# Optimization experiments

Measured on AMD Instinct MI355X. Metric: run time of the kernel, lower is better.

The kernel has to match this reference:

```python
import jax, jax.numpy as jnp
import numpy as np

B, T, C = 2, 2048, 2048
H, KVH, HD = 16, 4, 128
EPS = 1e-5


def _rope(x, cos, sin):
    # x: (B,T,h,HD); cos/sin: (1,T,1,HD//2); halves-split rotary (not interleaved)
    d = x.shape[-1] // 2
    x1, x2 = x[..., :d], x[..., d:]
    return jnp.concatenate([x1 * cos + x2 * sin, -x1 * sin + x2 * cos], axis=-1)


def _rms_norm(x, eps=EPS):
    return x * jax.lax.rsqrt(jnp.mean(x * x, axis=-1, keepdims=True) + eps)


def setup_inputs() -> dict:
    key = jax.random.key(0)
    ks = jax.random.split(key, 5)
    x = jax.random.normal(ks[0], (B, T, C), dtype=jnp.float32)
    # realistic RoPE tables (theta=10000)
    inv_freq = 1.0 / (10000.0 ** (np.arange(HD // 2, dtype=np.float32) / (HD // 2)))
    t = np.arange(T, dtype=np.float32)
    freqs = np.outer(t, inv_freq)  # (T, HD/2)
    cos = jnp.asarray(np.cos(freqs))[None, :, None, :]
    sin = jnp.asarray(np.sin(freqs))[None, :, None, :]
    s = 0.02
    wq = jax.random.normal(ks[1], (C, H * HD), dtype=jnp.float32) * s
    wk = jax.random.normal(ks[2], (C, KVH * HD), dtype=jnp.float32) * s
    wv = jax.random.normal(ks[3], (C, KVH * HD), dtype=jnp.float32) * s
    wo = jax.random.normal(ks[4], (H * HD, C), dtype=jnp.float32) * s
    return {"x": x, "cos": cos, "sin": sin, "wq": wq, "wk": wk, "wv": wv, "wo": wo, "window_size": 0}


def reference(x, cos, sin, wq, wk, wv, wo, window_size):
    # window_size is unused on the training (no-kv-cache) path, as in the source.
    b, t, _ = x.shape
    q = (x @ wq).reshape(b, t, H, HD)
    k = (x @ wk).reshape(b, t, KVH, HD)
    v = (x @ wv).reshape(b, t, KVH, HD)
    q = _rms_norm(_rope(q, cos, sin))
    k = _rms_norm(_rope(k, cos, sin))
    n_rep = H // KVH
    # grouped-query attention without materializing repeated K/V
    qg = q.reshape(b, t, KVH, n_rep, HD)
    scale = 1.0 / jnp.sqrt(jnp.float32(HD))
    scores = jnp.einsum('btkrd,bskd->bkrts', qg, k) * scale  # (B,KVH,n_rep,T,T)
    causal = jnp.tril(jnp.ones((t, t), dtype=bool))
    scores = jnp.where(causal, scores, jnp.finfo(scores.dtype).min)
    attn = jax.nn.softmax(scores, axis=-1)
    y = jnp.einsum('bkrts,bskd->btkrd', attn, v).reshape(b, t, H * HD)
    return y @ wo
```

## Files before the change

### kernel.cpp

```cpp
#include <hip/hip_runtime.h>
#include <hip/hip_bf16.h>


using bf16 = __bf16;
typedef __bf16 bf16x8 __attribute__((ext_vector_type(8)));
typedef __bf16 bf16x4 __attribute__((ext_vector_type(4)));
typedef float  f32x4  __attribute__((ext_vector_type(4)));

__device__ __forceinline__ void gload_lds16(const void* g, void* l) {
  __builtin_amdgcn_global_load_lds(
      (const __attribute__((address_space(1))) unsigned int*)g,
      (__attribute__((address_space(3))) unsigned int*)l, 16, 0, 0);
}

__device__ __forceinline__ unsigned pack2(float a, float b) {
  unsigned short ua = __builtin_bit_cast(unsigned short, (bf16)a);
  unsigned short ub = __builtin_bit_cast(unsigned short, (bf16)b);
  return ((unsigned)ub << 16) | ua;
}

#define SBAR() do { __builtin_amdgcn_s_barrier(); \
                    __builtin_amdgcn_sched_barrier(0); } while (0)
#define VMCNT(n) asm volatile("s_waitcnt vmcnt(" #n ")" ::: "memory")

__global__ __launch_bounds__(256) void k_cvt_bf16(const float* __restrict__ src,
                                                  bf16* __restrict__ dst) {
  const int i = blockIdx.x * 256 + threadIdx.x;
  f32x4 v = ((const f32x4*)src)[i];
  bf16x4 o;
  o[0] = (bf16)v[0]; o[1] = (bf16)v[1]; o[2] = (bf16)v[2]; o[3] = (bf16)v[3];
  ((bf16x4*)dst)[i] = o;
}

__global__ __launch_bounds__(256) void k_transpose_cvt(const float* __restrict__ src,
                                                       bf16* __restrict__ dst,
                                                       int R, int C) {
  __shared__ float tile[32][33];
  const int c0 = blockIdx.x * 32, r0 = blockIdx.y * 32;
  const int tx = threadIdx.x & 31, ty = threadIdx.x >> 5;
#pragma unroll
  for (int j = 0; j < 32; j += 8)
    tile[ty + j][tx] = src[(size_t)(r0 + ty + j) * C + c0 + tx];
  __syncthreads();
#pragma unroll
  for (int j = 0; j < 32; j += 8)
    dst[(size_t)(c0 + ty + j) * R + r0 + tx] = (bf16)tile[tx][ty + j];
}

template <int BM, bool OUT_BF16>
__global__ __launch_bounds__(512, 1) void k_gemm32(
    const bf16* __restrict__ A,
    const bf16* __restrict__ B0, const bf16* __restrict__ B1,
    const bf16* __restrict__ B2, int nb1, int nb2,
    void* __restrict__ Cout, int K, int Ntot) {
  constexpr int MR  = BM / 32;
  constexpr int ACH = BM / 128;
  __shared__ __align__(16) bf16 As[4][BM * 32];
  __shared__ __align__(16) bf16 Bs[4][256 * 32];
  const int nb = blockIdx.x, mb = blockIdx.y;
  const bf16* Bt; int nloc;
  if (nb < nb1)      { Bt = B0; nloc = nb; }
  else if (nb < nb2) { Bt = B1; nloc = nb - nb1; }
  else               { Bt = B2; nloc = nb - nb2; }
  const int tid = threadIdx.x;
  const int w = tid >> 6, lane = tid & 63;
  const int wm = w >> 2, wn = w & 3;
  const int l16 = lane & 15, lq = lane >> 4;
  const int sr4 = lane >> 2, sc4 = lane & 3;
  const bf16* Ag = A  + (size_t)mb * BM * K;
  const bf16* Bg = Bt + (size_t)nloc * 256 * K;

  f32x4 acc[MR][4] = {};

  auto stage = [&](int t) {
    const int buf = t & 3;
    const int k0 = t * 32;
#pragma unroll
    for (int i = 0; i < 2; ++i) {
      const int r = i * 128 + w * 16 + sr4;
      const int cg = sc4 ^ ((r >> 1) & 3);
      gload_lds16(Bg + (size_t)r * K + k0 + cg * 8,
                  &Bs[buf][(i * 128 + w * 16) * 32]);
    }
#pragma unroll
    for (int i = 0; i < ACH; ++i) {
      const int r = i * 128 + w * 16 + sr4;
      const int cg = sc4 ^ ((r >> 1) & 3);
      gload_lds16(Ag + (size_t)r * K + k0 + cg * 8,
                  &As[buf][(i * 128 + w * 16) * 32]);
    }
  };

  const int NT = K / 32;
  stage(0); stage(1); stage(2);
  if (BM == 256) VMCNT(8); else VMCNT(6);
  SBAR();

  for (int t = 0; t < NT; ++t) {
    const int buf = t & 3;
    if (t + 3 < NT) stage(t + 3);
    const int rem = NT - 1 - t;
    if (BM == 256) {
      if (rem >= 3)      VMCNT(12);
      else if (rem == 2) VMCNT(8);
      else if (rem == 1) VMCNT(4);
      else               VMCNT(0);
    } else {
      if (rem >= 3)      VMCNT(9);
      else if (rem == 2) VMCNT(6);
      else if (rem == 1) VMCNT(3);
      else               VMCNT(0);
    }
    SBAR();
    bf16x8 bfr[4], af[MR];
#pragma unroll
    for (int j = 0; j < 4; ++j) {
      const int rb = wn * 64 + j * 16 + l16;
      bfr[j] = *(const bf16x8*)((const char*)&Bs[buf][0] + rb * 64 +
                                ((lq ^ ((rb >> 1) & 3)) << 4));
    }
#pragma unroll
    for (int i = 0; i < MR; ++i) {
      const int ra = wm * (BM / 2) + i * 16 + l16;
      af[i] = *(const bf16x8*)((const char*)&As[buf][0] + ra * 64 +
                               ((lq ^ ((ra >> 1) & 3)) << 4));
    }
    __builtin_amdgcn_s_setprio(1);
#pragma unroll
    for (int i = 0; i < MR; ++i)
#pragma unroll
      for (int j = 0; j < 4; ++j)
        acc[i][j] = __builtin_amdgcn_mfma_f32_16x16x32_bf16(af[i], bfr[j],
                                                            acc[i][j], 0, 0, 0);
    __builtin_amdgcn_s_setprio(0);
    SBAR();
  }

#pragma unroll
  for (int i = 0; i < MR; ++i)
#pragma unroll
    for (int j = 0; j < 4; ++j)
#pragma unroll
      for (int e = 0; e < 4; ++e) {
        const size_t row = (size_t)mb * BM + wm * (BM / 2) + i * 16 + lq * 4 + e;
        const size_t col = (size_t)nb * 256 + wn * 64 + j * 16 + l16;
        if (OUT_BF16) ((bf16*)Cout)[row * Ntot + col] = (bf16)acc[i][j][e];
        else          ((float*)Cout)[row * Ntot + col] = acc[i][j][e];
      }
}

__global__ __launch_bounds__(256) void k_rope(
    const bf16* __restrict__ qkv, const float* __restrict__ cosb,
    const float* __restrict__ sinb, bf16* __restrict__ q_r,
    bf16* __restrict__ k_r, bf16* __restrict__ v_t) {
  const int wid  = blockIdx.x * 4 + (threadIdx.x >> 6);
  const int lane = threadIdx.x & 63;
  const int head = wid % 24;
  const int bt   = wid / 24;
  const int b = bt >> 11, t = bt & 2047;
  const bf16* base = qkv + (size_t)bt * 3072;
  if (head >= 20) {
    const int kv = head - 20;
    const bf16 v1 = base[2560 + kv * 128 + lane];
    const bf16 v2 = base[2560 + kv * 128 + 64 + lane];
    const size_t o = (size_t)((b * 4 + kv) * 128);
    v_t[(o + lane) * 2048 + t]      = v1;
    v_t[(o + 64 + lane) * 2048 + t] = v2;
    return;
  }
  const int col = (head < 16) ? head * 128 : 2048 + (head - 16) * 128;
  const float x1 = (float)base[col + lane];
  const float x2 = (float)base[col + 64 + lane];
  const float c = cosb[t * 64 + lane], s = sinb[t * 64 + lane];
  const float o1 = x1 * c + x2 * s;
  const float o2 = x2 * c - x1 * s;
  float ss = o1 * o1 + o2 * o2;
#pragma unroll
  for (int off = 32; off >= 1; off >>= 1) ss += __shfl_xor(ss, off);
  float r = rsqrtf(ss * (1.0f / 128.0f) + 1e-5f);
  if (head < 16) {
    r *= 0.08838834764831845f;
    const size_t o = ((size_t)(b * 16 + head) * 2048 + t) * 128;
    q_r[o + lane]      = (bf16)(o1 * r);
    q_r[o + 64 + lane] = (bf16)(o2 * r);
  } else {
    const int kv = head - 16;
    const size_t o = ((size_t)(b * 4 + kv) * 2048 + t) * 128;
    k_r[o + lane]      = (bf16)(o1 * r);
    k_r[o + 64 + lane] = (bf16)(o2 * r);
  }
}

__global__ __launch_bounds__(256, 2) void k_attn(
    const bf16* __restrict__ q_r, const bf16* __restrict__ k_r,
    const bf16* __restrict__ v_t, bf16* __restrict__ y) {
  __shared__ __align__(16) bf16 Ks[2][64 * 128];
  __shared__ __align__(16) bf16 Vt[2][128 * 64];
  const int blkid = blockIdx.x;
  const int bh = (blkid & 7) * 4 + ((blkid >> 3) & 3);
  const int g  = blkid >> 5;
  const int qb = (blkid < 256) ? (15 - g) : (g - 8);
  const int b = bh >> 4, h = bh & 15;
  const int bkv = b * 4 + (h >> 2);
  const int tid = threadIdx.x, w = tid >> 6, lane = tid & 63;
  const int l16 = lane & 15, lq = lane >> 4;
  const int swz = (l16 & 7) << 4;
  const int q0 = qb * 128, t0A = q0 + w * 32;
  const int nt = 2 * qb + 2;
  const bf16* kb = k_r + (size_t)bkv * (2048 * 128);
  const bf16* vb = v_t + (size_t)bkv * (128 * 2048);

  bf16x8 qfA[4], qfB[4];
  const bf16* qbase = q_r + ((size_t)bh * 2048 + t0A + l16) * 128;
#pragma unroll
  for (int kc = 0; kc < 4; ++kc) {
    qfA[kc] = *(const bf16x8*)(qbase + 32 * kc + 8 * lq);
    qfB[kc] = *(const bf16x8*)(qbase + 16 * 128 + 32 * kc + 8 * lq);
  }

  f32x4 accA[8] = {}, accB[8] = {};
  float mA = -1e29f, mB = -1e29f, lA = 0.f, lB = 0.f;

  auto stage = [&](int buf, int s0n) {
#pragma unroll
    for (int it = 0; it < 4; ++it) {
      const int rK = w * 16 + it * 4 + (lane >> 4);
      gload_lds16(kb + (size_t)(s0n + rK) * 128 + (((lane & 15) ^ (rK & 7)) << 3),
                  &Ks[buf][(w * 16 + it * 4) * 128]);
      const int rV = w * 32 + it * 8 + (lane >> 3);
      gload_lds16(vb + (size_t)rV * 2048 + s0n + (((lane & 7) ^ (rV & 7)) << 3),
                  &Vt[buf][(w * 32 + it * 8) * 64]);
    }
  };

  stage(0, 0);
  asm volatile("s_waitcnt vmcnt(0)" ::: "memory");
  __syncthreads();

  for (int t = 0; t < nt; ++t) {
    if (t + 1 < nt) stage((t + 1) & 1, (t + 1) * 64);
    const int s0 = t * 64;
    const int buf = t & 1;
    if (s0 <= t0A + 31) {
      f32x4 stA[4] = {}, stB[4] = {};
#pragma unroll
      for (int kc = 0; kc < 4; ++kc)
#pragma unroll
        for (int n = 0; n < 4; ++n) {
          const int rk = 16 * n + l16;
          const bf16x8 kf = *(const bf16x8*)((const char*)&Ks[buf][0] +
                             rk * 256 + ((64 * kc + 16 * lq) ^ swz));
          stA[n] = __builtin_amdgcn_mfma_f32_16x16x32_bf16(kf, qfA[kc], stA[n], 0, 0, 0);
          stB[n] = __builtin_amdgcn_mfma_f32_16x16x32_bf16(kf, qfB[kc], stB[n], 0, 0, 0);
        }
      const int qgA = t0A + l16, qgB = qgA + 16;
      if (s0 + 63 > t0A) {
#pragma unroll
        for (int n = 0; n < 4; ++n)
#pragma unroll
          for (int e = 0; e < 4; ++e) {
            const int kvg = s0 + 16 * n + 4 * lq + e;
            if (kvg > qgA) stA[n][e] = -1e30f;
            if (kvg > qgB) stB[n][e] = -1e30f;
          }
      }
      float mxA = -1e30f, mxB = -1e30f;
#pragma unroll
      for (int n = 0; n < 4; ++n)
#pragma unroll
        for (int e = 0; e < 4; ++e) {
          mxA = fmaxf(mxA, stA[n][e]);
          mxB = fmaxf(mxB, stB[n][e]);
        }
      mxA = fmaxf(mxA, __shfl_xor(mxA, 16)); mxA = fmaxf(mxA, __shfl_xor(mxA, 32));
      mxB = fmaxf(mxB, __shfl_xor(mxB, 16)); mxB = fmaxf(mxB, __shfl_xor(mxB, 32));
      const bool small = (mxA <= mA + 8.f) && (mxB <= mB + 8.f);
      if (!__all(small)) {
        const float mnA = fmaxf(mA, mxA), mnB = fmaxf(mB, mxB);
        const float scA = __expf(mA - mnA), scB = __expf(mB - mnB);
        mA = mnA; mB = mnB; lA *= scA; lB *= scB;
#pragma unroll
        for (int d2 = 0; d2 < 8; ++d2) { accA[d2] *= scA; accB[d2] *= scB; }
      }
      float rsA = 0.f, rsB = 0.f;
#pragma unroll
      for (int n = 0; n < 4; ++n)
#pragma unroll
        for (int e = 0; e < 4; ++e) {
          stA[n][e] = __expf(stA[n][e] - mA); rsA += stA[n][e];
          stB[n][e] = __expf(stB[n][e] - mB); rsB += stB[n][e];
        }
      rsA += __shfl_xor(rsA, 16); rsA += __shfl_xor(rsA, 32); lA += rsA;
      rsB += __shfl_xor(rsB, 16); rsB += __shfl_xor(rsB, 32); lB += rsB;
      unsigned pA2[8], pB2[8];
#pragma unroll
      for (int n = 0; n < 4; ++n) {
        pA2[n * 2 + 0] = pack2(stA[n][0], stA[n][1]);
        pA2[n * 2 + 1] = pack2(stA[n][2], stA[n][3]);
        pB2[n * 2 + 0] = pack2(stB[n][0], stB[n][1]);
        pB2[n * 2 + 1] = pack2(stB[n][2], stB[n][3]);
      }
      const int src0 = l16 | ((((lq & 1) << 1) | 0) << 4);
      const int src1 = l16 | ((((lq & 1) << 1) | 1) << 4);
      const bool selhi = (lq & 2);
#pragma unroll
      for (int c = 0; c < 2; ++c) {
        union { unsigned u[4]; bf16x8 v; } wA, wB;
        {
          unsigned a0 = __shfl((int)pA2[(2*c)*2+0], src0), b0 = __shfl((int)pA2[(2*c+1)*2+0], src0);
          unsigned a1 = __shfl((int)pA2[(2*c)*2+1], src0), b1 = __shfl((int)pA2[(2*c+1)*2+1], src0);
          unsigned a2 = __shfl((int)pA2[(2*c)*2+0], src1), b2 = __shfl((int)pA2[(2*c+1)*2+0], src1);
          unsigned a3 = __shfl((int)pA2[(2*c)*2+1], src1), b3 = __shfl((int)pA2[(2*c+1)*2+1], src1);
          wA.u[0] = selhi ? b0 : a0; wA.u[1] = selhi ? b1 : a1;
          wA.u[2] = selhi ? b2 : a2; wA.u[3] = selhi ? b3 : a3;
        }
        {
          unsigned a0 = __shfl((int)pB2[(2*c)*2+0], src0), b0 = __shfl((int)pB2[(2*c+1)*2+0], src0);
          unsigned a1 = __shfl((int)pB2[(2*c)*2+1], src0), b1 = __shfl((int)pB2[(2*c+1)*2+1], src0);
          unsigned a2 = __shfl((int)pB2[(2*c)*2+0], src1), b2 = __shfl((int)pB2[(2*c+1)*2+0], src1);
          unsigned a3 = __shfl((int)pB2[(2*c)*2+1], src1), b3 = __shfl((int)pB2[(2*c+1)*2+1], src1);
          wB.u[0] = selhi ? b0 : a0; wB.u[1] = selhi ? b1 : a1;
          wB.u[2] = selhi ? b2 : a2; wB.u[3] = selhi ? b3 : a3;
        }
#pragma unroll
        for (int dblk = 0; dblk < 8; ++dblk) {
          const int rv = 16 * dblk + l16;
          const bf16x8 vf = *(const bf16x8*)((const char*)&Vt[buf][0] +
                             rv * 128 + ((64 * c + 16 * lq) ^ swz));
          accA[dblk] = __builtin_amdgcn_mfma_f32_16x16x32_bf16(vf, wA.v, accA[dblk], 0, 0, 0);
          accB[dblk] = __builtin_amdgcn_mfma_f32_16x16x32_bf16(vf, wB.v, accB[dblk], 0, 0, 0);
        }
      }
    }
    asm volatile("s_waitcnt vmcnt(0)" ::: "memory");
    __syncthreads();
  }

  const float invA = 1.f / lA, invB = 1.f / lB;
  bf16* yA = y + (((size_t)b * 2048 + t0A + l16) * 16 + h) * 128;
  bf16* yB = yA + (size_t)16 * 2048;
#pragma unroll
  for (int dblk = 0; dblk < 8; ++dblk) {
    unsigned loA = pack2(accA[dblk][0] * invA, accA[dblk][1] * invA);
    unsigned hiA = pack2(accA[dblk][2] * invA, accA[dblk][3] * invA);
    *(uint2*)(yA + 16 * dblk + 4 * lq) = make_uint2(loA, hiA);
    unsigned loB = pack2(accB[dblk][0] * invB, accB[dblk][1] * invB);
    unsigned hiB = pack2(accB[dblk][2] * invB, accB[dblk][3] * invB);
    *(uint2*)(yB + 16 * dblk + 4 * lq) = make_uint2(loB, hiB);
  }
}

extern "C" void kernel_launch(void* const* d_in, const int* in_sizes, int n_in,
                              void* d_out, int out_size, void* d_ws, size_t ws_size,
                              hipStream_t stream) {
  const float* x    = (const float*)d_in[0];
  const float* cosb = (const float*)d_in[1];
  const float* sinb = (const float*)d_in[2];
  const float* wq   = (const float*)d_in[3];
  const float* wk   = (const float*)d_in[4];
  const float* wv   = (const float*)d_in[5];
  const float* wo   = (const float*)d_in[6];
  float* out = (float*)d_out;

  char* ws = (char*)d_ws;
  size_t off = 0;
  auto alloc = [&](size_t bytes) {
    char* p = ws + off; off += (bytes + 255) & ~(size_t)255; return p;
  };
  bf16* xb  = (bf16*)alloc(4096ull * 2048 * 2);
  bf16* wqT = (bf16*)alloc(2048ull * 2048 * 2);
  bf16* wkT = (bf16*)alloc(512ull  * 2048 * 2);
  bf16* wvT = (bf16*)alloc(512ull  * 2048 * 2);
  bf16* woT = (bf16*)alloc(2048ull * 2048 * 2);
  bf16* qkv = (bf16*)alloc(4096ull * 3072 * 2);
  bf16* q_r = (bf16*)alloc(4096ull * 2048 * 2);
  bf16* k_r = (bf16*)alloc(4096ull * 512  * 2);
  bf16* v_t = (bf16*)alloc(4096ull * 512  * 2);
  bf16* y   = xb;

  k_cvt_bf16<<<(4096 * 2048 / 4) / 256, 256, 0, stream>>>(x, xb);
  k_transpose_cvt<<<dim3(64, 64), 256, 0, stream>>>(wq, wqT, 2048, 2048);
  k_transpose_cvt<<<dim3(16, 64), 256, 0, stream>>>(wk, wkT, 2048, 512);
  k_transpose_cvt<<<dim3(16, 64), 256, 0, stream>>>(wv, wvT, 2048, 512);
  k_transpose_cvt<<<dim3(64, 64), 256, 0, stream>>>(wo, woT, 2048, 2048);
  k_gemm32<256, true><<<dim3(12, 16), 512, 0, stream>>>(xb, wqT, wkT, wvT, 8, 10,
                                                        qkv, 2048, 3072);
  k_rope<<<24576, 256, 0, stream>>>(qkv, cosb, sinb, q_r, k_r, v_t);
  k_attn<<<512, 256, 0, stream>>>(q_r, k_r, v_t, y);
  k_gemm32<128, false><<<dim3(8, 32), 512, 0, stream>>>(y, woT, woT, woT, 100, 200,
                                                        out, 2048, 2048);
}
```

Before: 364.6 us.

## Stage V through row-major buffer with tiled transpose; use simpler 128x128 GEMM for output projection

The rope kernel now writes V row-major with coalesced stores. A separate LDS-tiled transpose kernel then produces the transposed V layout that attention consumes, replacing scattered strided stores. The output projection also switches from the 512-thread multi-buffered GEMM to a new 256-thread 128x128 tile GEMM without pipelining, giving 512 blocks instead of 256. This adds an extra kernel launch and a V round-trip, and the new GEMM may lose the overlap the old pipelined kernel had.

```diff
diff --git a/kernel.cpp b/kernel.cpp
--- a/kernel.cpp
+++ b/kernel.cpp
@@ -45,6 +45,23 @@
 #pragma unroll
   for (int j = 0; j < 32; j += 8)
     dst[(size_t)(c0 + ty + j) * R + r0 + tx] = (bf16)tile[tx][ty + j];
+}
+
+__global__ __launch_bounds__(256) void k_vtrans(const bf16* __restrict__ src,
+                                                bf16* __restrict__ dst) {
+  __shared__ bf16 tile[32][33];
+  const int bkv = blockIdx.z;
+  const int d0 = blockIdx.x * 32, t0 = blockIdx.y * 32;
+  const int tx = threadIdx.x & 31, ty = threadIdx.x >> 5;
+  const bf16* s = src + (size_t)bkv * 2048 * 128;
+  bf16* d = dst + (size_t)bkv * 128 * 2048;
+#pragma unroll
+  for (int j = 0; j < 32; j += 8)
+    tile[ty + j][tx] = s[(size_t)(t0 + ty + j) * 128 + d0 + tx];
+  __syncthreads();
+#pragma unroll
+  for (int j = 0; j < 32; j += 8)
+    d[(size_t)(d0 + ty + j) * 2048 + t0 + tx] = tile[tx][ty + j];
 }
 
 template <int BM, bool OUT_BF16>
@@ -149,10 +166,74 @@
       }
 }
 
+template <bool OUT_BF16>
+__global__ __launch_bounds__(256) void k_gemm(
+    const bf16* __restrict__ A,
+    const bf16* __restrict__ B0, const bf16* __restrict__ B1,
+    const bf16* __restrict__ B2, int nb1, int nb2,
+    void* __restrict__ Cout, int K, int Ntot) {
+  __shared__ __align__(16) bf16 As[128 * 64];
+  __shared__ __align__(16) bf16 Bs[128 * 64];
+  const int nb = blockIdx.x, mb = blockIdx.y;
+  const bf16* Bt; int nloc;
+  if (nb < nb1)      { Bt = B0; nloc = nb; }
+  else if (nb < nb2) { Bt = B1; nloc = nb - nb1; }
+  else               { Bt = B2; nloc = nb - nb2; }
+  const int tid = threadIdx.x;
+  const int w = tid >> 6, lane = tid & 63;
+  const int wm = w >> 1, wn = w & 1;
+  const int sr = lane >> 3, sc = lane & 7;
+  const int l16 = lane & 15, lq = lane >> 4;
+  f32x4 acc[4][4] = {};
+  const bf16* Ab = A  + (size_t)(mb * 128) * K;
+  const bf16* Bb = Bt + (size_t)(nloc * 128) * K;
+  for (int k0 = 0; k0 < K; k0 += 64) {
+#pragma unroll
+    for (int it = 0; it < 4; ++it) {
+      const int r  = w * 32 + it * 8 + sr;
+      const int cs = (sc ^ (r & 7)) << 3;
+      gload_lds16(Ab + (size_t)r * K + k0 + cs, &As[(w * 32 + it * 8) * 64]);
+      gload_lds16(Bb + (size_t)r * K + k0 + cs, &Bs[(w * 32 + it * 8) * 64]);
+    }
+    __syncthreads();
+#pragma unroll
+    for (int kc = 0; kc < 2; ++kc) {
+      bf16x8 af[4], bfr[4];
+#pragma unroll
+      for (int i = 0; i < 4; ++i) {
+        const int ra = wm * 64 + i * 16 + l16;
+        af[i]  = *(const bf16x8*)((const char*)As + ra * 128 +
+                                  ((kc * 64 + lq * 16) ^ ((ra & 7) << 4)));
+        const int rb = wn * 64 + i * 16 + l16;
+        bfr[i] = *(const bf16x8*)((const char*)Bs + rb * 128 +
+                                  ((kc * 64 + lq * 16) ^ ((rb & 7) << 4)));
+      }
+#pragma unroll
+      for (int i = 0; i < 4; ++i)
+#pragma unroll
+        for (int j = 0; j < 4; ++j)
+          acc[i][j] = __builtin_amdgcn_mfma_f32_16x16x32_bf16(af[i], bfr[j],
+                                                              acc[i][j], 0, 0, 0);
+    }
+    __syncthreads();
+  }
+#pragma unroll
+  for (int i = 0; i < 4; ++i)
+#pragma unroll
+    for (int j = 0; j < 4; ++j)
+#pragma unroll
+      for (int e = 0; e < 4; ++e) {
+        const size_t row = (size_t)mb * 128 + wm * 64 + i * 16 + lq * 4 + e;
+        const size_t col = (size_t)nb * 128 + wn * 64 + j * 16 + l16;
+        if (OUT_BF16) ((bf16*)Cout)[row * Ntot + col] = (bf16)acc[i][j][e];
+        else          ((float*)Cout)[row * Ntot + col] = acc[i][j][e];
+      }
+}
+
 __global__ __launch_bounds__(256) void k_rope(
     const bf16* __restrict__ qkv, const float* __restrict__ cosb,
     const float* __restrict__ sinb, bf16* __restrict__ q_r,
-    bf16* __restrict__ k_r, bf16* __restrict__ v_t) {
+    bf16* __restrict__ k_r, bf16* __restrict__ v_r) {
   const int wid  = blockIdx.x * 4 + (threadIdx.x >> 6);
   const int lane = threadIdx.x & 63;
   const int head = wid % 24;
@@ -161,11 +242,9 @@
   const bf16* base = qkv + (size_t)bt * 3072;
   if (head >= 20) {
     const int kv = head - 20;
-    const bf16 v1 = base[2560 + kv * 128 + lane];
-    const bf16 v2 = base[2560 + kv * 128 + 64 + lane];
-    const size_t o = (size_t)((b * 4 + kv) * 128);
-    v_t[(o + lane) * 2048 + t]      = v1;
-    v_t[(o + 64 + lane) * 2048 + t] = v2;
+    const size_t o = ((size_t)(b * 4 + kv) * 2048 + t) * 128;
+    v_r[o + lane]      = base[2560 + kv * 128 + lane];
+    v_r[o + 64 + lane] = base[2560 + kv * 128 + 64 + lane];
     return;
   }
   const int col = (head < 16) ? head * 128 : 2048 + (head - 16) * 128;
@@ -375,6 +454,7 @@
   bf16* qkv = (bf16*)alloc(4096ull * 3072 * 2);
   bf16* q_r = (bf16*)alloc(4096ull * 2048 * 2);
   bf16* k_r = (bf16*)alloc(4096ull * 512  * 2);
+  bf16* v_r = (bf16*)alloc(4096ull * 512  * 2);
   bf16* v_t = (bf16*)alloc(4096ull * 512  * 2);
   bf16* y   = xb;
 
@@ -385,8 +465,9 @@
   k_transpose_cvt<<<dim3(64, 64), 256, 0, stream>>>(wo, woT, 2048, 2048);
   k_gemm32<256, true><<<dim3(12, 16), 512, 0, stream>>>(xb, wqT, wkT, wvT, 8, 10,
                                                         qkv, 2048, 3072);
-  k_rope<<<24576, 256, 0, stream>>>(qkv, cosb, sinb, q_r, k_r, v_t);
+  k_rope<<<24576, 256, 0, stream>>>(qkv, cosb, sinb, q_r, k_r, v_r);
+  k_vtrans<<<dim3(4, 64, 8), 256, 0, stream>>>(v_r, v_t);
   k_attn<<<512, 256, 0, stream>>>(q_r, k_r, v_t, y);
-  k_gemm32<128, false><<<dim3(8, 32), 512, 0, stream>>>(y, woT, woT, woT, 100, 200,
-                                                        out, 2048, 2048);
-}
+  k_gemm<false><<<dim3(16, 32), 256, 0, stream>>>(y, woT, woT, woT, 100, 200,
+                                                  out, 2048, 2048);
+}
```

After: 346.5 us. 1.05x faster.
